# Optimization experiments

Hardware: AMD Instinct MI355X
Metric: run time of the kernel (lower is better)

## Reference

```python
import jax, jax.numpy as jnp
import numpy as np

C = 128; HEADS = 4; DH = C // HEADS; R = 8; EPS = 1e-5; SCALE = DH ** -0.5
B = 1; H = 32; W = 32; D = 32


def _rel_index(r):
    # Faithful replication of RelativePositionBias index (incl. its quirks:
    # depth coord never offset, only coord0 scaled, negative indices wrap).
    coords = np.stack(np.meshgrid(np.arange(r), np.arange(r), np.arange(r), indexing='ij'))
    flat = coords.reshape(3, -1)
    rel = (flat[:, :, None] - flat[:, None, :]).transpose(1, 2, 0).astype(np.int64)
    rel[:, :, 0] += r - 1
    rel[:, :, 1] += r - 1
    rel[:, :, 0] *= 2 * r - 1
    idx = rel.sum(-1)
    tbl = (2 * r - 1) ** 3
    return np.where(idx < 0, idx + tbl, idx)  # torch-style negative index wrap

REL_IDX = jnp.array(_rel_index(R))  # [R^3, R^3]


def _interp_matrix(n_in, n_out):
    # 1-D linear interpolation matrix, align_corners=True (trilinear is separable)
    pos = np.arange(n_out) * (n_in - 1) / (n_out - 1)
    lo = np.clip(np.floor(pos).astype(np.int64), 0, n_in - 2)
    w = (pos - lo).astype(np.float32)
    M = np.zeros((n_out, n_in), np.float32)
    M[np.arange(n_out), lo] = 1.0 - w
    M[np.arange(n_out), lo + 1] += w
    return jnp.array(M)


def _conv3d(x, w, groups=1):
    ks = w.shape[-1]; p = ks // 2
    return jax.lax.conv_general_dilated(
        x, w, (1, 1, 1), ((p, p),) * 3,
        dimension_numbers=('NCDHW', 'OIDHW', 'NCDHW'),
        feature_group_count=groups)


def _bn(x, g, b):
    # training-mode BatchNorm3d: batch stats over (N, spatial), biased var
    mu = x.mean(axis=(0, 2, 3, 4), keepdims=True)
    var = x.var(axis=(0, 2, 3, 4), keepdims=True)
    return (x - mu) * jax.lax.rsqrt(var + EPS) * g.reshape(1, -1, 1, 1, 1) + b.reshape(1, -1, 1, 1, 1)


def _block(x, bn1_g, bn1_b, qkv_dw, qkv_pw, rel_table, out_dw, out_pw, bn2_g, bn2_b, mlp_w):
    Bx, Cx, Hx, Wx, Dx = x.shape
    h = _bn(x, bn1_g, bn1_b)
    qkv = _conv3d(_conv3d(h, qkv_dw, groups=C), qkv_pw)
    q, k, v = jnp.split(qkv, 3, axis=1)
    # trilinear downsample k, v to (R, R, R), align_corners=True
    Mh, Mw, Md = _interp_matrix(Hx, R), _interp_matrix(Wx, R), _interp_matrix(Dx, R)
    k = jnp.einsum('bchwd,ph,qw,rd->bcpqr', k, Mh, Mw, Md)
    v = jnp.einsum('bchwd,ph,qw,rd->bcpqr', v, Mh, Mw, Md)
    # channel layout is (dim_head, heads)
    q = q.reshape(Bx, DH, HEADS, Hx * Wx * Dx).transpose(0, 2, 3, 1)  # b h N d
    k = k.reshape(Bx, DH, HEADS, R ** 3).transpose(0, 2, 3, 1)       # b h M d
    v = v.reshape(Bx, DH, HEADS, R ** 3).transpose(0, 2, 3, 1)
    attn = jnp.einsum('bhid,bhjd->bhij', q, k)
    # relative position bias, expanded by repeat_interleave on each spatial axis
    bias = rel_table[REL_IDX]                          # [R^3, R^3, heads]
    bias = bias.reshape(R, R, R, R ** 3, HEADS)
    ih = jnp.arange(Hx) // (Hx // R)
    iw = jnp.arange(Wx) // (Wx // R)
    idd = jnp.arange(Dx) // (Dx // R)
    bias = bias[ih][:, iw][:, :, idd]                  # [H, W, D, M, heads]
    bias = bias.reshape(Hx * Wx * Dx, R ** 3, HEADS).transpose(2, 0, 1)[None]  # [1, h, N, M]
    attn = (attn + bias) * SCALE                        # scale AFTER bias add, as in source
    attn = jax.nn.softmax(attn, axis=-1)
    out = jnp.einsum('bhij,bhjd->bhid', attn, v)        # b h N d
    out = out.transpose(0, 3, 1, 2).reshape(Bx, C, Hx, Wx, Dx)  # (dim_head heads) channels
    out = _conv3d(_conv3d(out, out_dw, groups=C), out_pw)
    out = out + x
    residue = out
    out = jax.nn.relu(_bn(out, bn2_g, bn2_b))
    out = _conv3d(out, mlp_w)  # 1x1x1, no bias
    return out + residue


def setup_inputs() -> dict:
    key = jax.random.key(0)
    ks = jax.random.split(key, 12)
    s = 0.02
    return {
        'x': jax.random.normal(ks[0], (B, C, H, W, D), jnp.float32),
        'bn1_g': jnp.ones((C,), jnp.float32),
        'bn1_b': jnp.zeros((C,), jnp.float32),
        'qkv_dw': jax.random.normal(ks[1], (C, 1, 3, 3, 3), jnp.float32) * s,
        'qkv_pw': jax.random.normal(ks[2], (3 * C, C, 1, 1, 1), jnp.float32) * s,
        'rel_table': jax.random.normal(ks[3], ((2 * R - 1) ** 3, HEADS), jnp.float32) * s,
        'out_dw': jax.random.normal(ks[4], (C, 1, 3, 3, 3), jnp.float32) * s,
        'out_pw': jax.random.normal(ks[5], (C, C, 1, 1, 1), jnp.float32) * s,
        'bn2_g': jnp.ones((C,), jnp.float32),
        'bn2_b': jnp.zeros((C,), jnp.float32),
        'mlp_w': jax.random.normal(ks[6], (C, C, 1, 1, 1), jnp.float32) * s,
    }


def reference(x, bn1_g, bn1_b, qkv_dw, qkv_pw, rel_table, out_dw, out_pw, bn2_g, bn2_b, mlp_w):
    return _block(x, bn1_g, bn1_b, qkv_dw, qkv_pw, rel_table, out_dw, out_pw, bn2_g, bn2_b, mlp_w)
```

## Files before the change

kernel.cpp:

```cpp
#include <hip/hip_runtime.h>
#include <math.h>


typedef short bf16x8 __attribute__((ext_vector_type(8)));
typedef float f32x4 __attribute__((ext_vector_type(4)));
typedef unsigned short u16x8 __attribute__((ext_vector_type(8)));

constexpr int CNUM  = 128;
constexpr int NSP   = 32768;
constexpr int HEADS = 4;
constexpr int M3    = 512;
constexpr float EPSV  = 1e-5f;
constexpr float SCALE = 0.17677669529663688f;
constexpr float SK    = SCALE * 1.44269504088896340736f;

constexpr size_t F_HDW16 = 0;
constexpr size_t F_HDWT  = 2097152;
constexpr size_t F_QKV   = 4194304;
constexpr size_t F_ATTN  = 0;
constexpr size_t F_TMP2  = F_QKV;
constexpr size_t F_TMP2T = F_QKV + 2097152;
constexpr size_t F_Y1    = F_QKV + 4194304;
constexpr size_t F_Y1T   = F_QKV + 8388608;
constexpr size_t F_KD    = 16777216;
constexpr size_t F_VT    = F_KD + 32768;
constexpr size_t F_BIAS  = F_VT + 32768;
constexpr size_t F_ST    = F_BIAS + 524288;

__device__ inline ushort f2bf(float f) {
  unsigned u = __float_as_uint(f);
  u += 0x7fff + ((u >> 16) & 1);
  return (ushort)(u >> 16);
}
__device__ inline float bf2f(ushort u) { return __uint_as_float(((unsigned)u) << 16); }

__global__ __launch_bounds__(256) void bn_stats(
    const float* __restrict__ x, const float* __restrict__ g,
    const float* __restrict__ bb, float* __restrict__ scale,
    float* __restrict__ shift) {
  const int c = blockIdx.x;
  const float4* p = (const float4*)(x + (size_t)c * NSP);
  float s = 0.f, s2 = 0.f;
  for (int i = threadIdx.x; i < NSP / 4; i += 256) {
    float4 v = p[i];
    s  += v.x + v.y + v.z + v.w;
    s2 += v.x * v.x + v.y * v.y + v.z * v.z + v.w * v.w;
  }
  __shared__ float rs[4], rs2[4];
  for (int off = 32; off > 0; off >>= 1) {
    s  += __shfl_down(s, off);
    s2 += __shfl_down(s2, off);
  }
  if ((threadIdx.x & 63) == 0) { rs[threadIdx.x >> 6] = s; rs2[threadIdx.x >> 6] = s2; }
  __syncthreads();
  if (threadIdx.x == 0) {
    float S = rs[0] + rs[1] + rs[2] + rs[3];
    float S2 = rs2[0] + rs2[1] + rs2[2] + rs2[3];
    float mu = S / (float)NSP;
    float var = S2 / (float)NSP - mu * mu;
    float sc = g[c] * rsqrtf(var + EPSV);
    scale[c] = sc;
    shift[c] = bb[c] - mu * sc;
  }
}

template <bool AFFINE>
__global__ __launch_bounds__(256) void dwconv3(
    const float* __restrict__ in, const float* __restrict__ w27,
    const float* __restrict__ scale, const float* __restrict__ shift,
    ushort* __restrict__ out) {
  const int idx = blockIdx.x * 256 + threadIdx.x;
  const int d0 = (idx & 3) << 3;
  const int ww = (idx >> 2) & 31;
  const int hh = (idx >> 7) & 31;
  const int c  = idx >> 12;
  const float sc = AFFINE ? scale[c] : 1.f;
  const float sh = AFFINE ? shift[c] : 0.f;
  const float* pc = in + ((size_t)c << 15);
  const float* wc = w27 + c * 27;
  float wreg[27];
#pragma unroll
  for (int k = 0; k < 27; ++k) wreg[k] = wc[k];

  float acc[8] = {};
#pragma unroll
  for (int a = 0; a < 3; ++a) {
    int h2 = hh + a - 1;
    if ((unsigned)h2 > 31u) continue;
#pragma unroll
    for (int b = 0; b < 3; ++b) {
      int w2 = ww + b - 1;
      if ((unsigned)w2 > 31u) continue;
      const float* row = pc + (h2 << 10) + (w2 << 5) + d0;
      float4 v0 = *(const float4*)(row);
      float4 v1 = *(const float4*)(row + 4);
      float win[10];
      if (AFFINE) {
        win[1] = fmaf(v0.x, sc, sh); win[2] = fmaf(v0.y, sc, sh);
        win[3] = fmaf(v0.z, sc, sh); win[4] = fmaf(v0.w, sc, sh);
        win[5] = fmaf(v1.x, sc, sh); win[6] = fmaf(v1.y, sc, sh);
        win[7] = fmaf(v1.z, sc, sh); win[8] = fmaf(v1.w, sc, sh);
        win[0] = (d0 > 0)  ? fmaf(row[-1], sc, sh) : 0.f;
        win[9] = (d0 < 24) ? fmaf(row[8],  sc, sh) : 0.f;
      } else {
        win[1] = v0.x; win[2] = v0.y; win[3] = v0.z; win[4] = v0.w;
        win[5] = v1.x; win[6] = v1.y; win[7] = v1.z; win[8] = v1.w;
        win[0] = (d0 > 0)  ? row[-1] : 0.f;
        win[9] = (d0 < 24) ? row[8]  : 0.f;
      }
      const float w0 = wreg[(a * 3 + b) * 3 + 0];
      const float w1 = wreg[(a * 3 + b) * 3 + 1];
      const float w2v = wreg[(a * 3 + b) * 3 + 2];
#pragma unroll
      for (int j = 0; j < 8; ++j)
        acc[j] += w0 * win[j] + w1 * win[j + 1] + w2v * win[j + 2];
    }
  }
  u16x8 o;
#pragma unroll
  for (int j = 0; j < 8; ++j) o[j] = f2bf(acc[j]);
  *(u16x8*)(out + ((size_t)c << 15) + (hh << 10) + (ww << 5) + d0) = o;
}

template <int MODE>
__global__ __launch_bounds__(256) void transpose_cn(
    const void* __restrict__ inp, const float* __restrict__ sc_,
    const float* __restrict__ sh_, ushort* __restrict__ outp) {
  __shared__ ushort T[64][72];
  const int tid = threadIdx.x;
  const int c0 = (blockIdx.x & 1) << 6;
  const int n0 = (blockIdx.x >> 1) << 6;
  const int r = tid >> 2, q = (tid & 3) << 4;
  if (MODE == 0) {
    const ushort* src = (const ushort*)inp + (size_t)(c0 + r) * NSP + n0 + q;
    *(u16x8*)&T[r][q]     = *(const u16x8*)src;
    *(u16x8*)&T[r][q + 8] = *(const u16x8*)(src + 8);
  } else {
    const float* src = (const float*)inp + (size_t)(c0 + r) * NSP + n0 + q;
    const float s = sc_[c0 + r], h = sh_[c0 + r];
    float4 v0 = ((const float4*)src)[0], v1 = ((const float4*)src)[1];
    float4 v2 = ((const float4*)src)[2], v3 = ((const float4*)src)[3];
    u16x8 a, b;
    a[0] = f2bf(fmaxf(fmaf(v0.x, s, h), 0.f));
    a[1] = f2bf(fmaxf(fmaf(v0.y, s, h), 0.f));
    a[2] = f2bf(fmaxf(fmaf(v0.z, s, h), 0.f));
    a[3] = f2bf(fmaxf(fmaf(v0.w, s, h), 0.f));
    a[4] = f2bf(fmaxf(fmaf(v1.x, s, h), 0.f));
    a[5] = f2bf(fmaxf(fmaf(v1.y, s, h), 0.f));
    a[6] = f2bf(fmaxf(fmaf(v1.z, s, h), 0.f));
    a[7] = f2bf(fmaxf(fmaf(v1.w, s, h), 0.f));
    b[0] = f2bf(fmaxf(fmaf(v2.x, s, h), 0.f));
    b[1] = f2bf(fmaxf(fmaf(v2.y, s, h), 0.f));
    b[2] = f2bf(fmaxf(fmaf(v2.z, s, h), 0.f));
    b[3] = f2bf(fmaxf(fmaf(v2.w, s, h), 0.f));
    b[4] = f2bf(fmaxf(fmaf(v3.x, s, h), 0.f));
    b[5] = f2bf(fmaxf(fmaf(v3.y, s, h), 0.f));
    b[6] = f2bf(fmaxf(fmaf(v3.z, s, h), 0.f));
    b[7] = f2bf(fmaxf(fmaf(v3.w, s, h), 0.f));
    *(u16x8*)&T[r][q]     = a;
    *(u16x8*)&T[r][q + 8] = b;
  }
  __syncthreads();
  const int rn = tid >> 2, cq = (tid & 3) << 4;
  u16x8 o0, o1;
#pragma unroll
  for (int j = 0; j < 8; ++j) { o0[j] = T[cq + j][rn]; o1[j] = T[cq + 8 + j][rn]; }
  ushort* dst = outp + (size_t)(n0 + rn) * 128 + c0 + cq;
  *(u16x8*)dst       = o0;
  *(u16x8*)(dst + 8) = o1;
}

template <bool RES>
__global__ __launch_bounds__(256) void gemm_mfma(
    const float* __restrict__ W, const ushort* __restrict__ Bt,
    const float* __restrict__ res, float* __restrict__ out) {
  __shared__ ushort Wl[128][40];
  __shared__ ushort Bl[128][40];
  const int tid = threadIdx.x;
  const int lane = tid & 63, w = tid >> 6;
  const int g = lane >> 4, c = lane & 15;
  const int n0 = blockIdx.x << 7, oc0 = blockIdx.y << 7;
  const int wr = (w >> 1) << 6, wc = (w & 1) << 6;
  f32x4 acc[4][4];
#pragma unroll
  for (int mt = 0; mt < 4; ++mt)
#pragma unroll
    for (int nt = 0; nt < 4; ++nt) acc[mt][nt] = {0.f, 0.f, 0.f, 0.f};
  const int sr = tid >> 1, sh2 = (tid & 1) << 4;
  for (int k0 = 0; k0 < 128; k0 += 32) {
    __syncthreads();
    {
      const float* wsrc = W + (size_t)(oc0 + sr) * 128 + k0 + sh2;
      float4 a = ((const float4*)wsrc)[0];
      float4 b = ((const float4*)wsrc)[1];
      float4 cc = ((const float4*)wsrc)[2];
      float4 dd = ((const float4*)wsrc)[3];
      u16x8 p0, p1;
      p0[0] = f2bf(a.x);  p0[1] = f2bf(a.y);  p0[2] = f2bf(a.z);  p0[3] = f2bf(a.w);
      p0[4] = f2bf(b.x);  p0[5] = f2bf(b.y);  p0[6] = f2bf(b.z);  p0[7] = f2bf(b.w);
      p1[0] = f2bf(cc.x); p1[1] = f2bf(cc.y); p1[2] = f2bf(cc.z); p1[3] = f2bf(cc.w);
      p1[4] = f2bf(dd.x); p1[5] = f2bf(dd.y); p1[6] = f2bf(dd.z); p1[7] = f2bf(dd.w);
      *(u16x8*)&Wl[sr][sh2]     = p0;
      *(u16x8*)&Wl[sr][sh2 + 8] = p1;
      const ushort* bsrc = Bt + (size_t)(n0 + sr) * 128 + k0 + sh2;
      *(u16x8*)&Bl[sr][sh2]     = *(const u16x8*)bsrc;
      *(u16x8*)&Bl[sr][sh2 + 8] = *(const u16x8*)(bsrc + 8);
    }
    __syncthreads();
    bf16x8 af[4], bfr[4];
#pragma unroll
    for (int mt = 0; mt < 4; ++mt)
      af[mt] = *(const bf16x8*)&Wl[wr + mt * 16 + c][g * 8];
#pragma unroll
    for (int nt = 0; nt < 4; ++nt)
      bfr[nt] = *(const bf16x8*)&Bl[wc + nt * 16 + c][g * 8];
#pragma unroll
    for (int mt = 0; mt < 4; ++mt)
#pragma unroll
      for (int nt = 0; nt < 4; ++nt)
        acc[mt][nt] = __builtin_amdgcn_mfma_f32_16x16x32_bf16(
            af[mt], bfr[nt], acc[mt][nt], 0, 0, 0);
  }
#pragma unroll
  for (int mt = 0; mt < 4; ++mt) {
#pragma unroll
    for (int nt = 0; nt < 4; ++nt) {
      const int n = n0 + wc + nt * 16 + c;
#pragma unroll
      for (int r = 0; r < 4; ++r) {
        const int oc = oc0 + wr + mt * 16 + g * 4 + r;
        size_t off = (size_t)oc * NSP + n;
        float o = acc[mt][nt][r];
        if (RES) o += res[off];
        out[off] = o;
      }
    }
  }
}

__device__ inline void interp8(int p, int& lo, float& w) {
  double pos = (double)p * 31.0 / 7.0;
  int l = (int)pos;
  if (l > 30) l = 30;
  lo = l;
  w = (float)(pos - (double)l);
}

__global__ __launch_bounds__(128) void downsample_kv(
    const float* __restrict__ qkv, ushort* __restrict__ kd,
    ushort* __restrict__ vt) {
  const int m = blockIdx.x, c = threadIdx.x;
  const int p = m >> 6, q = (m >> 3) & 7, r = m & 7;
  int lp, lq, lr; float wp, wq, wr;
  interp8(p, lp, wp); interp8(q, lq, wq); interp8(r, lr, wr);
  const float* kp = qkv + (size_t)(CNUM + c) * NSP;
  const float* vp = qkv + (size_t)(2 * CNUM + c) * NSP;
  float ak = 0.f, av = 0.f;
#pragma unroll
  for (int a = 0; a < 2; ++a)
#pragma unroll
    for (int b = 0; b < 2; ++b)
#pragma unroll
      for (int e = 0; e < 2; ++e) {
        float wgt = (a ? wp : 1.f - wp) * (b ? wq : 1.f - wq) * (e ? wr : 1.f - wr);
        int off = ((lp + a) << 10) + ((lq + b) << 5) + (lr + e);
        ak = fmaf(wgt, kp[off], ak);
        av = fmaf(wgt, vp[off], av);
      }
  const int d = c >> 2, h = c & 3;
  kd[((size_t)(h * M3 + m)) * 32 + d] = f2bf(ak);
  vt[((size_t)(h * 32 + d)) * M3 + m] = f2bf(av);
}

__global__ __launch_bounds__(256) void build_bias(
    const float* __restrict__ rel, ushort* __restrict__ biasmat) {
  const int nr = blockIdx.x;
  const int p0 = nr >> 6, q0 = (nr >> 3) & 7, r0 = nr & 7;
  for (int m = threadIdx.x; m < M3; m += 256) {
    int p1 = m >> 6, q1 = (m >> 3) & 7, r1 = m & 7;
    int idx = (p0 - p1 + 7) * 15 + (q0 - q1 + 7) + (r0 - r1);
    if (idx < 0) idx += 3375;
#pragma unroll
    for (int h = 0; h < 4; ++h)
      biasmat[((size_t)(h * M3 + nr)) * M3 + m] = f2bf(rel[idx * 4 + h]);
  }
}

__global__ __launch_bounds__(256, 2) void attention_mfma(
    const float* __restrict__ q, const ushort* __restrict__ kd,
    const ushort* __restrict__ vt, const ushort* __restrict__ biasg,
    float* __restrict__ attn_out) {
  __shared__ ushort lds[31040];
  ushort* Kl = lds;
  ushort* Vl = lds + 5120;
  ushort* Bl = lds + 9472;
  ushort* Pl = lds + 13632;
  const int tid = threadIdx.x;
  const int lane = tid & 63, w = tid >> 6;
  const int g = lane >> 4, c = lane & 15;
  const int head = blockIdx.x >> 8;
  const int n0 = (blockIdx.x & 255) << 7;

  {
    int nr_base = ((n0 >> 12) << 6) + ((((n0 >> 5) & 31) >> 2) << 3);
    int row = tid >> 5, col = (tid & 31) << 4;
    const float4* src =
        (const float4*)(biasg + ((size_t)(head * M3 + nr_base + row)) * M3 + col);
    *(float4*)&Bl[row * 520 + col] = src[0];
    *(float4*)&Bl[row * 520 + col + 8] = src[1];
  }

  bf16x8 qf[2];
#pragma unroll
  for (int s = 0; s < 2; ++s) {
    int n = n0 + w * 32 + s * 16 + c;
#pragma unroll
    for (int j = 0; j < 8; ++j)
      qf[s][j] = (short)f2bf(q[(size_t)((g * 8 + j) * 4 + head) * NSP + n]);
  }

  f32x4 acc[2][2];
#pragma unroll
  for (int s = 0; s < 2; ++s)
#pragma unroll
    for (int dt = 0; dt < 2; ++dt) acc[s][dt] = {0.f, 0.f, 0.f, 0.f};
  float rmax[2] = {-1e30f, -1e30f};
  float rsum[2] = {0.f, 0.f};
  ushort* Pw = Pl + w * 2 * 2176;
  const f32x4 zero4 = {0.f, 0.f, 0.f, 0.f};

  for (int mt = 0; mt < M3; mt += 128) {
    __syncthreads();
    {
      int r = tid >> 1, hp = (tid & 1) << 4;
      const float4* ksrc =
          (const float4*)(kd + ((size_t)(head * M3 + mt + r)) * 32 + hp);
      *(float4*)&Kl[r * 40 + hp] = ksrc[0];
      *(float4*)&Kl[r * 40 + hp + 8] = ksrc[1];
      int d = tid >> 3, mc = (tid & 7) << 4;
      const float4* vs = (const float4*)(vt + ((size_t)(head * 32 + d)) * M3 + mt + mc);
      *(float4*)&Vl[d * 136 + mc] = vs[0];
      *(float4*)&Vl[d * 136 + mc + 8] = vs[1];
    }
    __syncthreads();
    f32x4 st[2][8];
#pragma unroll
    for (int t = 0; t < 8; ++t) {
      bf16x8 kf = *(const bf16x8*)&Kl[(t * 16 + c) * 40 + g * 8];
      st[0][t] = __builtin_amdgcn_mfma_f32_16x16x32_bf16(kf, qf[0], zero4, 0, 0, 0);
      st[1][t] = __builtin_amdgcn_mfma_f32_16x16x32_bf16(kf, qf[1], zero4, 0, 0, 0);
    }
#pragma unroll
    for (int s = 0; s < 2; ++s) {
      const int brow = s * 4 + (c >> 2);
      float mx = -1e30f;
#pragma unroll
      for (int t = 0; t < 8; ++t) {
        ushort4 bb = *(const ushort4*)&Bl[brow * 520 + mt + t * 16 + g * 4];
        st[s][t][0] = (st[s][t][0] + bf2f(bb.x)) * SK;
        st[s][t][1] = (st[s][t][1] + bf2f(bb.y)) * SK;
        st[s][t][2] = (st[s][t][2] + bf2f(bb.z)) * SK;
        st[s][t][3] = (st[s][t][3] + bf2f(bb.w)) * SK;
        mx = fmaxf(mx, fmaxf(fmaxf(st[s][t][0], st[s][t][1]),
                             fmaxf(st[s][t][2], st[s][t][3])));
      }
      mx = fmaxf(mx, __shfl_xor(mx, 16));
      mx = fmaxf(mx, __shfl_xor(mx, 32));
      float mnew = fmaxf(rmax[s], mx);
      float f = exp2f(rmax[s] - mnew);
      rmax[s] = mnew;
      float psum = 0.f;
      ushort* Ps = Pw + s * 2176;
#pragma unroll
      for (int t = 0; t < 8; ++t) {
        float p0 = exp2f(st[s][t][0] - mnew);
        float p1 = exp2f(st[s][t][1] - mnew);
        float p2 = exp2f(st[s][t][2] - mnew);
        float p3 = exp2f(st[s][t][3] - mnew);
        psum += (p0 + p1) + (p2 + p3);
        ushort4 pw4;
        pw4.x = f2bf(p0); pw4.y = f2bf(p1); pw4.z = f2bf(p2); pw4.w = f2bf(p3);
        *(ushort4*)&Ps[c * 136 + t * 16 + g * 4] = pw4;
      }
      psum += __shfl_xor(psum, 16);
      psum += __shfl_xor(psum, 32);
      rsum[s] = rsum[s] * f + psum;
      float fr0 = __shfl(f, g * 4 + 0), fr1 = __shfl(f, g * 4 + 1);
      float fr2 = __shfl(f, g * 4 + 2), fr3 = __shfl(f, g * 4 + 3);
#pragma unroll
      for (int dt = 0; dt < 2; ++dt) {
        acc[s][dt][0] *= fr0; acc[s][dt][1] *= fr1;
        acc[s][dt][2] *= fr2; acc[s][dt][3] *= fr3;
      }
    }
#pragma unroll
    for (int ks = 0; ks < 4; ++ks) {
      bf16x8 pa0 = *(const bf16x8*)&Pw[c * 136 + ks * 32 + g * 8];
      bf16x8 pa1 = *(const bf16x8*)&Pw[2176 + c * 136 + ks * 32 + g * 8];
#pragma unroll
      for (int dt = 0; dt < 2; ++dt) {
        bf16x8 vb = *(const bf16x8*)&Vl[(dt * 16 + c) * 136 + ks * 32 + g * 8];
        acc[0][dt] = __builtin_amdgcn_mfma_f32_16x16x32_bf16(pa0, vb, acc[0][dt], 0, 0, 0);
        acc[1][dt] = __builtin_amdgcn_mfma_f32_16x16x32_bf16(pa1, vb, acc[1][dt], 0, 0, 0);
      }
    }
  }
  __syncthreads();
  float* Ol = (float*)Pl;
#pragma unroll
  for (int s = 0; s < 2; ++s) {
    float inv = 1.f / rsum[s];
#pragma unroll
    for (int r = 0; r < 4; ++r) {
      float fr = __shfl(inv, g * 4 + r);
      int row = w * 32 + s * 16 + g * 4 + r;
#pragma unroll
      for (int dt = 0; dt < 2; ++dt)
        Ol[row * 33 + dt * 16 + c] = acc[s][dt][r] * fr;
    }
  }
  __syncthreads();
  {
    int d = tid >> 3, seg = tid & 7;
    float vals[16];
#pragma unroll
    for (int i = 0; i < 16; ++i) vals[i] = Ol[(seg * 16 + i) * 33 + d];
    float* dst = attn_out + (size_t)(d * 4 + head) * NSP + n0 + seg * 16;
#pragma unroll
    for (int i = 0; i < 4; ++i) *(float4*)(dst + i * 4) = *(float4*)&vals[i * 4];
  }
}

extern "C" void kernel_launch(void* const* d_in, const int* in_sizes, int n_in,
                              void* d_out, int out_size, void* d_ws, size_t ws_size,
                              hipStream_t stream) {
  (void)in_sizes; (void)n_in; (void)out_size; (void)ws_size;
  const float* x      = (const float*)d_in[0];
  const float* bn1_g  = (const float*)d_in[1];
  const float* bn1_b  = (const float*)d_in[2];
  const float* qkv_dw = (const float*)d_in[3];
  const float* qkv_pw = (const float*)d_in[4];
  const float* rel    = (const float*)d_in[5];
  const float* out_dw = (const float*)d_in[6];
  const float* out_pw = (const float*)d_in[7];
  const float* bn2_g  = (const float*)d_in[8];
  const float* bn2_b  = (const float*)d_in[9];
  const float* mlp_w  = (const float*)d_in[10];
  float* out = (float*)d_out;
  float* ws = (float*)d_ws;

  ushort* hdw16 = (ushort*)(ws + F_HDW16);
  ushort* hdwt  = (ushort*)(ws + F_HDWT);
  float*  qkv   = ws + F_QKV;
  float*  attn_o = ws + F_ATTN;
  ushort* tmp2  = (ushort*)(ws + F_TMP2);
  ushort* tmp2t = (ushort*)(ws + F_TMP2T);
  float*  y1    = ws + F_Y1;
  ushort* y1t   = (ushort*)(ws + F_Y1T);
  ushort* kdb   = (ushort*)(ws + F_KD);
  ushort* vtb   = (ushort*)(ws + F_VT);
  ushort* bias  = (ushort*)(ws + F_BIAS);
  float* sc1 = ws + F_ST, *sh1 = sc1 + 128, *sc2 = sh1 + 128, *sh2 = sc2 + 128;

  bn_stats<<<128, 256, 0, stream>>>(x, bn1_g, bn1_b, sc1, sh1);
  dwconv3<true><<<2048, 256, 0, stream>>>(x, qkv_dw, sc1, sh1, hdw16);
  transpose_cn<0><<<1024, 256, 0, stream>>>(hdw16, nullptr, nullptr, hdwt);
  gemm_mfma<false><<<dim3(256, 3), 256, 0, stream>>>(qkv_pw, hdwt, nullptr, qkv);
  downsample_kv<<<M3, 128, 0, stream>>>(qkv, kdb, vtb);
  build_bias<<<M3, 256, 0, stream>>>(rel, bias);
  attention_mfma<<<HEADS * 256, 256, 0, stream>>>(qkv, kdb, vtb, bias, attn_o);
  dwconv3<false><<<2048, 256, 0, stream>>>(attn_o, out_dw, nullptr, nullptr, tmp2);
  transpose_cn<0><<<1024, 256, 0, stream>>>(tmp2, nullptr, nullptr, tmp2t);
  gemm_mfma<true><<<dim3(256, 1), 256, 0, stream>>>(out_pw, tmp2t, x, y1);
  bn_stats<<<128, 256, 0, stream>>>(y1, bn2_g, bn2_b, sc2, sh2);
  transpose_cn<1><<<1024, 256, 0, stream>>>(y1, sc2, sh2, y1t);
  gemm_mfma<true><<<dim3(256, 1), 256, 0, stream>>>(mlp_w, y1t, y1, out);
}
```

Baseline: 262.5 us.

## Shrink attention LDS via interleaved softmax/PV chunks, prescale bias, raise occupancy

```diff
diff --git a/kernel.cpp b/kernel.cpp
--- a/kernel.cpp
+++ b/kernel.cpp
@@ -282,15 +282,15 @@
     if (idx < 0) idx += 3375;
 #pragma unroll
     for (int h = 0; h < 4; ++h)
-      biasmat[((size_t)(h * M3 + nr)) * M3 + m] = f2bf(rel[idx * 4 + h]);
-  }
-}
-
-__global__ __launch_bounds__(256, 2) void attention_mfma(
+      biasmat[((size_t)(h * M3 + nr)) * M3 + m] = f2bf(rel[idx * 4 + h] * SK);
+  }
+}
+
+__global__ __launch_bounds__(256, 4) void attention_mfma(
     const float* __restrict__ q, const ushort* __restrict__ kd,
     const ushort* __restrict__ vt, const ushort* __restrict__ biasg,
     float* __restrict__ attn_out) {
-  __shared__ ushort lds[31040];
+  __shared__ ushort lds[16192];
   ushort* Kl = lds;
   ushort* Vl = lds + 5120;
   ushort* Bl = lds + 9472;
@@ -326,7 +326,7 @@
     for (int dt = 0; dt < 2; ++dt) acc[s][dt] = {0.f, 0.f, 0.f, 0.f};
   float rmax[2] = {-1e30f, -1e30f};
   float rsum[2] = {0.f, 0.f};
-  ushort* Pw = Pl + w * 2 * 2176;
+  ushort* Pw = Pl + w * 640;
   const f32x4 zero4 = {0.f, 0.f, 0.f, 0.f};
 
   for (int mt = 0; mt < M3; mt += 128) {
@@ -344,12 +344,14 @@
     }
     __syncthreads();
     f32x4 st[2][8];
+    __builtin_amdgcn_s_setprio(1);
 #pragma unroll
     for (int t = 0; t < 8; ++t) {
       bf16x8 kf = *(const bf16x8*)&Kl[(t * 16 + c) * 40 + g * 8];
       st[0][t] = __builtin_amdgcn_mfma_f32_16x16x32_bf16(kf, qf[0], zero4, 0, 0, 0);
       st[1][t] = __builtin_amdgcn_mfma_f32_16x16x32_bf16(kf, qf[1], zero4, 0, 0, 0);
     }
+    __builtin_amdgcn_s_setprio(0);
 #pragma unroll
     for (int s = 0; s < 2; ++s) {
       const int brow = s * 4 + (c >> 2);
@@ -357,10 +359,10 @@
 #pragma unroll
       for (int t = 0; t < 8; ++t) {
         ushort4 bb = *(const ushort4*)&Bl[brow * 520 + mt + t * 16 + g * 4];
-        st[s][t][0] = (st[s][t][0] + bf2f(bb.x)) * SK;
-        st[s][t][1] = (st[s][t][1] + bf2f(bb.y)) * SK;
-        st[s][t][2] = (st[s][t][2] + bf2f(bb.z)) * SK;
-        st[s][t][3] = (st[s][t][3] + bf2f(bb.w)) * SK;
+        st[s][t][0] = fmaf(st[s][t][0], SK, bf2f(bb.x));
+        st[s][t][1] = fmaf(st[s][t][1], SK, bf2f(bb.y));
+        st[s][t][2] = fmaf(st[s][t][2], SK, bf2f(bb.z));
+        st[s][t][3] = fmaf(st[s][t][3], SK, bf2f(bb.w));
         mx = fmaxf(mx, fmaxf(fmaxf(st[s][t][0], st[s][t][1]),
                              fmaxf(st[s][t][2], st[s][t][3])));
       }
@@ -369,44 +371,46 @@
       float mnew = fmaxf(rmax[s], mx);
       float f = exp2f(rmax[s] - mnew);
       rmax[s] = mnew;
+      float fr0 = __shfl(f, g * 4 + 0), fr1 = __shfl(f, g * 4 + 1);
+      float fr2 = __shfl(f, g * 4 + 2), fr3 = __shfl(f, g * 4 + 3);
+#pragma unroll
+      for (int dt = 0; dt < 2; ++dt) {
+        acc[s][dt][0] *= fr0; acc[s][dt][1] *= fr1;
+        acc[s][dt][2] *= fr2; acc[s][dt][3] *= fr3;
+      }
       float psum = 0.f;
-      ushort* Ps = Pw + s * 2176;
-#pragma unroll
-      for (int t = 0; t < 8; ++t) {
-        float p0 = exp2f(st[s][t][0] - mnew);
-        float p1 = exp2f(st[s][t][1] - mnew);
-        float p2 = exp2f(st[s][t][2] - mnew);
-        float p3 = exp2f(st[s][t][3] - mnew);
-        psum += (p0 + p1) + (p2 + p3);
-        ushort4 pw4;
-        pw4.x = f2bf(p0); pw4.y = f2bf(p1); pw4.z = f2bf(p2); pw4.w = f2bf(p3);
-        *(ushort4*)&Ps[c * 136 + t * 16 + g * 4] = pw4;
+#pragma unroll
+      for (int ks = 0; ks < 4; ++ks) {
+#pragma unroll
+        for (int dt2 = 0; dt2 < 2; ++dt2) {
+          const int t = ks * 2 + dt2;
+          float p0 = exp2f(st[s][t][0] - mnew);
+          float p1 = exp2f(st[s][t][1] - mnew);
+          float p2 = exp2f(st[s][t][2] - mnew);
+          float p3 = exp2f(st[s][t][3] - mnew);
+          psum += (p0 + p1) + (p2 + p3);
+          unsigned lo, hi;
+          asm("v_cvt_pk_bf16_f32 %0, %1, %2" : "=v"(lo) : "v"(p0), "v"(p1));
+          asm("v_cvt_pk_bf16_f32 %0, %1, %2" : "=v"(hi) : "v"(p2), "v"(p3));
+          uint2 pk; pk.x = lo; pk.y = hi;
+          *(uint2*)&Pw[c * 40 + dt2 * 16 + g * 4] = pk;
+        }
+        bf16x8 pa = *(const bf16x8*)&Pw[c * 40 + g * 8];
+        __builtin_amdgcn_s_setprio(1);
+#pragma unroll
+        for (int dt = 0; dt < 2; ++dt) {
+          bf16x8 vb = *(const bf16x8*)&Vl[(dt * 16 + c) * 136 + ks * 32 + g * 8];
+          acc[s][dt] = __builtin_amdgcn_mfma_f32_16x16x32_bf16(pa, vb, acc[s][dt], 0, 0, 0);
+        }
+        __builtin_amdgcn_s_setprio(0);
       }
       psum += __shfl_xor(psum, 16);
       psum += __shfl_xor(psum, 32);
       rsum[s] = rsum[s] * f + psum;
-      float fr0 = __shfl(f, g * 4 + 0), fr1 = __shfl(f, g * 4 + 1);
-      float fr2 = __shfl(f, g * 4 + 2), fr3 = __shfl(f, g * 4 + 3);
-#pragma unroll
-      for (int dt = 0; dt < 2; ++dt) {
-        acc[s][dt][0] *= fr0; acc[s][dt][1] *= fr1;
-        acc[s][dt][2] *= fr2; acc[s][dt][3] *= fr3;
-      }
-    }
-#pragma unroll
-    for (int ks = 0; ks < 4; ++ks) {
-      bf16x8 pa0 = *(const bf16x8*)&Pw[c * 136 + ks * 32 + g * 8];
-      bf16x8 pa1 = *(const bf16x8*)&Pw[2176 + c * 136 + ks * 32 + g * 8];
-#pragma unroll
-      for (int dt = 0; dt < 2; ++dt) {
-        bf16x8 vb = *(const bf16x8*)&Vl[(dt * 16 + c) * 136 + ks * 32 + g * 8];
-        acc[0][dt] = __builtin_amdgcn_mfma_f32_16x16x32_bf16(pa0, vb, acc[0][dt], 0, 0, 0);
-        acc[1][dt] = __builtin_amdgcn_mfma_f32_16x16x32_bf16(pa1, vb, acc[1][dt], 0, 0, 0);
-      }
     }
   }
   __syncthreads();
-  float* Ol = (float*)Pl;
+  float* Ol = (float*)lds;
 #pragma unroll
   for (int s = 0; s < 2; ++s) {
     float inv = 1.f / rsum[s];
```

Result: slower. 270.7 us (+3.2%).
